# Performance work log

Hardware: AMD Instinct MI355X
Metric: run time of the kernel (lower is better)

Reference implementation:

```python
import jax, jax.numpy as jnp
import numpy as np

B, L, DM, H = 1, 2048, 3072, 24
D = DM // H            # 128 head dim
MLP = 4 * DM           # 12288
EPS = 1e-6


def setup_inputs() -> dict:
    key = jax.random.key(0)
    ks = jax.random.split(key, 12)
    s = lambda fan_in: 1.0 / np.sqrt(fan_in)
    return {
        "x": jax.random.normal(ks[0], (B, L, DM), jnp.float32),
        "vec": jax.random.normal(ks[1], (B, DM), jnp.float32),
        "pe": jax.random.normal(ks[2], (1, 1, L, D // 2, 2, 2), jnp.float32),
        # Modulation linear: dim -> 3*dim
        "mod_w": jax.random.normal(ks[3], (DM, 3 * DM), jnp.float32) * s(DM),
        "mod_b": jnp.zeros((3 * DM,), jnp.float32),
        # linear1: dim -> 3*dim + mlp
        "lin1_w": jax.random.normal(ks[4], (DM, 3 * DM + MLP), jnp.float32) * s(DM),
        "lin1_b": jnp.zeros((3 * DM + MLP,), jnp.float32),
        # linear2: dim + mlp -> dim
        "lin2_w": jax.random.normal(ks[5], (DM + MLP, DM), jnp.float32) * s(DM + MLP),
        "lin2_b": jnp.zeros((DM,), jnp.float32),
        # QKNorm RMS scales (per head_dim)
        "q_scale": jnp.ones((D,), jnp.float32),
        "k_scale": jnp.ones((D,), jnp.float32),
    }


def _rms_norm(t, scale):
    # RMSNorm over last dim (head_dim), eps 1e-6
    rrms = jax.lax.rsqrt(jnp.mean(jnp.square(t), axis=-1, keepdims=True) + EPS)
    return t * rrms * scale


def _apply_rope(t, pe):
    # t: (B,H,L,D); pe: (1,1,L,D/2,2,2) as in flux apply_rope
    t2 = t.reshape(B, H, L, D // 2, 1, 2)
    out = pe[..., 0] * t2[..., 0] + pe[..., 1] * t2[..., 1]  # (B,H,L,D/2,2)
    return out.reshape(B, H, L, D)


def reference(x, vec, pe, mod_w, mod_b, lin1_w, lin1_b, lin2_w, lin2_b, q_scale, k_scale):
    # Modulation: Linear(silu(vec)) -> shift, scale, gate, each (B,1,DM)
    mod = jax.nn.silu(vec) @ mod_w + mod_b
    shift, scale, gate = jnp.split(mod[:, None, :], 3, axis=-1)

    # pre_norm: LayerNorm without affine, eps 1e-6
    mu = jnp.mean(x, axis=-1, keepdims=True)
    var = jnp.mean(jnp.square(x - mu), axis=-1, keepdims=True)
    xn = (x - mu) * jax.lax.rsqrt(var + EPS)
    x_mod = (1.0 + scale) * xn + shift

    # fused QKV + MLP projection
    h = x_mod @ lin1_w + lin1_b
    qkv, mlp = h[..., : 3 * DM], h[..., 3 * DM :]
    qkv = qkv.reshape(B, L, 3, H, D).transpose(2, 0, 3, 1, 4)  # (3,B,H,L,D)
    q, k, v = qkv[0], qkv[1], qkv[2]

    q = _rms_norm(q, q_scale)
    k = _rms_norm(k, k_scale)
    q = _apply_rope(q, pe)
    k = _apply_rope(k, pe)

    # scaled dot-product attention (non-causal, SDPA default scale)
    scores = jnp.einsum("bhqd,bhkd->bhqk", q, k) * (1.0 / np.sqrt(D))
    attn = jax.nn.softmax(scores, axis=-1)
    o = jnp.einsum("bhqk,bhkd->bhqd", attn, v)
    o = o.transpose(0, 2, 1, 3).reshape(B, L, DM)  # B H L D -> B L (H D)

    out = jnp.concatenate([o, jax.nn.gelu(mlp, approximate=True)], axis=-1) @ lin2_w + lin2_b
    return x + gate * out
```

## Files before the change

### kernel.cpp

```cpp
#include <hip/hip_runtime.h>
#include <math.h>

#define LQ 2048
#define DMODEL 3072
#define NHEADS 24
#define DHEADC 128
#define NQKV 9216
#define NOUT1 21504
#define KIN2 15360
#define EPSV 1e-6f

typedef __attribute__((ext_vector_type(8))) short short8;
typedef __attribute__((ext_vector_type(4))) short short4v;
typedef __attribute__((ext_vector_type(4))) float f32x4;

__device__ __forceinline__ short f2bf(float f) {
  unsigned int u = __float_as_uint(f);
  unsigned int r = (u + 0x7fffu + ((u >> 16) & 1u)) >> 16;
  return (short)(unsigned short)r;
}

__device__ __forceinline__ float geluf(float v) {
  float inner = 0.7978845608028654f * (v + 0.044715f * v * v * v);
  return 0.5f * v * (1.0f + tanhf(inner));
}

__device__ __forceinline__ void async_ld16(void* lds, const void* g) {
  __builtin_amdgcn_global_load_lds(
      (const __attribute__((address_space(1))) unsigned int*)g,
      (__attribute__((address_space(3))) unsigned int*)lds, 16, 0, 0);
}

__global__ __launch_bounds__(256) void k_wconv(const float* __restrict__ w,
                                               short* __restrict__ wt,
                                               int K, int N) {
  __shared__ float tile[32][33];
  int bk = blockIdx.x * 32, bn = blockIdx.y * 32;
  int t = threadIdx.x;
  int r = t >> 3, c = (t & 7) * 4;
  float4 v = *reinterpret_cast<const float4*>(w + (size_t)(bk + r) * N + bn + c);
  tile[r][c + 0] = v.x; tile[r][c + 1] = v.y; tile[r][c + 2] = v.z; tile[r][c + 3] = v.w;
  __syncthreads();
  short4v o;
  o[0] = f2bf(tile[c + 0][r]); o[1] = f2bf(tile[c + 1][r]);
  o[2] = f2bf(tile[c + 2][r]); o[3] = f2bf(tile[c + 3][r]);
  *reinterpret_cast<short4v*>(wt + (size_t)(bn + r) * K + bk + c) = o;
}

__global__ __launch_bounds__(256) void k_modpart(const float* __restrict__ vec,
                                                 const float* __restrict__ mod_w,
                                                 float* __restrict__ partial) {
  __shared__ float sv[128];
  int t = threadIdx.x;
  int nb = blockIdx.x * 256;
  int kb = blockIdx.y * 128;
  if (t < 128) { float z = vec[kb + t]; sv[t] = z / (1.0f + expf(-z)); }
  __syncthreads();
  const float* wp = mod_w + (size_t)kb * NQKV + nb + t;
  float acc = 0.0f;
#pragma unroll 8
  for (int k = 0; k < 128; k++) acc += sv[k] * wp[(size_t)k * NQKV];
  partial[(size_t)blockIdx.y * NQKV + nb + t] = acc;
}

__global__ __launch_bounds__(256) void k_modred(const float* __restrict__ partial,
                                                const float* __restrict__ mod_b,
                                                float* __restrict__ modv) {
  int n = blockIdx.x * 256 + threadIdx.x;
  float acc = mod_b[n];
#pragma unroll
  for (int ky = 0; ky < 24; ky++) acc += partial[(size_t)ky * NQKV + n];
  modv[n] = acc;
}

__global__ __launch_bounds__(256) void k_ln(const float* __restrict__ x,
                                            const float* __restrict__ modv,
                                            short* __restrict__ xmod) {
  int l = blockIdx.x, t = threadIdx.x;
  const float* xr = x + (size_t)l * DMODEL;
  const float4* xr4 = (const float4*)xr;
  float4 vbuf[3];
  float s = 0.f, ss = 0.f;
#pragma unroll
  for (int i = 0; i < 3; i++) {
    float4 v = xr4[t + i * 256];
    vbuf[i] = v;
    s += v.x + v.y + v.z + v.w;
    ss += v.x * v.x + v.y * v.y + v.z * v.z + v.w * v.w;
  }
#pragma unroll
  for (int m = 32; m >= 1; m >>= 1) { s += __shfl_xor(s, m); ss += __shfl_xor(ss, m); }
  __shared__ float red[8];
  __shared__ float stats[2];
  int wave = t >> 6;
  if ((t & 63) == 0) { red[wave] = s; red[4 + wave] = ss; }
  __syncthreads();
  if (t == 0) {
    float st = red[0] + red[1] + red[2] + red[3];
    float sst = red[4] + red[5] + red[6] + red[7];
    float mu = st / DMODEL;
    float var = sst / DMODEL - mu * mu;
    stats[0] = mu; stats[1] = rsqrtf(var + EPSV);
  }
  __syncthreads();
  float mu = stats[0], rr = stats[1];
#pragma unroll
  for (int i = 0; i < 3; i++) {
    float4 v = vbuf[i];
    int c = (t + i * 256) * 4;
    short4v o;
    o[0] = f2bf((1.f + modv[DMODEL + c + 0]) * ((v.x - mu) * rr) + modv[c + 0]);
    o[1] = f2bf((1.f + modv[DMODEL + c + 1]) * ((v.y - mu) * rr) + modv[c + 1]);
    o[2] = f2bf((1.f + modv[DMODEL + c + 2]) * ((v.z - mu) * rr) + modv[c + 2]);
    o[3] = f2bf((1.f + modv[DMODEL + c + 3]) * ((v.w - mu) * rr) + modv[c + 3]);
    *(short4v*)(xmod + (size_t)l * DMODEL + c) = o;
  }
}

__global__ __launch_bounds__(256) void k_gemm1(const short* __restrict__ A,
                                               const short* __restrict__ Bt,
                                               const float* __restrict__ bias,
                                               float* __restrict__ qraw,
                                               float* __restrict__ kraw,
                                               short* __restrict__ vt,
                                               short* __restrict__ a2) {
  __shared__ __align__(16) short As[128 * 32];
  __shared__ __align__(16) short Bs[128 * 32];
  const int K = DMODEL;
  int t = threadIdx.x;
  int bm = blockIdx.x * 128, bn = blockIdx.y * 128;
  int wave = t >> 6, lane = t & 63;
  int wm = (wave >> 1) * 64, wn = (wave & 1) * 64;
  int lrow = lane & 15, lko = (lane >> 4) * 8;
  int srow = wave * 16 + (lane >> 2);
  int scol = (lane & 3) * 8;
  const short* ga0 = A + (size_t)(bm + srow) * K + scol;
  const short* ga1 = ga0 + (size_t)64 * K;
  const short* gb0 = Bt + (size_t)(bn + srow) * K + scol;
  const short* gb1 = gb0 + (size_t)64 * K;
  short* la0 = As + wave * 512;
  short* la1 = As + 64 * 32 + wave * 512;
  short* lb0 = Bs + wave * 512;
  short* lb1 = Bs + 64 * 32 + wave * 512;
  f32x4 zero = {0.f, 0.f, 0.f, 0.f};
  f32x4 acc[4][4];
#pragma unroll
  for (int i = 0; i < 4; i++)
#pragma unroll
    for (int j = 0; j < 4; j++) acc[i][j] = zero;
  for (int k0 = 0; k0 < K; k0 += 32) {
    __syncthreads();
    async_ld16(la0, ga0 + k0);
    async_ld16(la1, ga1 + k0);
    async_ld16(lb0, gb0 + k0);
    async_ld16(lb1, gb1 + k0);
    __syncthreads();
    short8 af[4], bfr[4];
#pragma unroll
    for (int i = 0; i < 4; i++) af[i] = *(const short8*)&As[(wm + i * 16 + lrow) * 32 + lko];
#pragma unroll
    for (int j = 0; j < 4; j++) bfr[j] = *(const short8*)&Bs[(wn + j * 16 + lrow) * 32 + lko];
#pragma unroll
    for (int i = 0; i < 4; i++)
#pragma unroll
      for (int j = 0; j < 4; j++)
        acc[i][j] = __builtin_amdgcn_mfma_f32_16x16x32_bf16(af[i], bfr[j], acc[i][j], 0, 0, 0);
  }
  int r0 = bm + wm + ((lane >> 4) << 2);
  int c0 = bn + wn + lrow;
#pragma unroll
  for (int j = 0; j < 4; j++) {
    int col = c0 + j * 16;
    float bb = bias[col];
#pragma unroll
    for (int i = 0; i < 4; i++) {
#pragma unroll
      for (int r = 0; r < 4; r++) {
        float v = acc[i][j][r] + bb;
        int row = r0 + i * 16 + r;
        if (col < NQKV) {
          int s = col / DMODEL;
          int rem = col - s * DMODEL;
          int hh = rem >> 7, d = rem & 127;
          if (s == 0)      qraw[((size_t)hh * LQ + row) * DHEADC + d] = v;
          else if (s == 1) kraw[((size_t)hh * LQ + row) * DHEADC + d] = v;
          else             vt[((size_t)hh * DHEADC + d) * LQ + row] = f2bf(v);
        } else {
          a2[(size_t)row * KIN2 + DMODEL + (col - NQKV)] = f2bf(geluf(v));
        }
      }
    }
  }
}

__global__ __launch_bounds__(256) void k_qkprep(const float* __restrict__ qraw,
                                                const float* __restrict__ kraw,
                                                const float* __restrict__ pe,
                                                const float* __restrict__ q_scale,
                                                const float* __restrict__ k_scale,
                                                short* __restrict__ qn,
                                                short* __restrict__ kn) {
  int wave = threadIdx.x >> 6, lane = threadIdx.x & 63;
  int l = blockIdx.x * 4 + wave;
  int h = blockIdx.y;
  int isK = blockIdx.z;
  const float* src = (isK ? kraw : qraw) + ((size_t)h * LQ + l) * DHEADC;
  const float* sc  = isK ? k_scale : q_scale;
  short* dst = (isK ? kn : qn) + ((size_t)h * LQ + l) * DHEADC;
  float2 tv = *(const float2*)(src + lane * 2);
  float ssq = tv.x * tv.x + tv.y * tv.y;
#pragma unroll
  for (int m = 1; m < 64; m <<= 1) ssq += __shfl_xor(ssq, m);
  float rr = rsqrtf(ssq * (1.0f / 128.0f) + EPSV);
  float t0 = tv.x * rr * sc[lane * 2];
  float t1 = tv.y * rr * sc[lane * 2 + 1];
  float4 p4 = *(const float4*)(pe + ((size_t)l * 64 + lane) * 4);
  float o0 = p4.x * t0 + p4.y * t1;
  float o1 = p4.z * t0 + p4.w * t1;
  if (!isK) { o0 *= 0.08838834764831845f; o1 *= 0.08838834764831845f; }
  dst[lane * 2] = f2bf(o0);
  dst[lane * 2 + 1] = f2bf(o1);
}

__global__ __launch_bounds__(256) void k_flash(const short* __restrict__ qn,
                                               const short* __restrict__ kn,
                                               const short* __restrict__ vt,
                                               short* __restrict__ a2) {
  __shared__ short Qs[128][136];
  __shared__ short Ks[32][136];
  __shared__ short Vs[128][40];
  __shared__ short Ps[4][32][40];
  int t = threadIdx.x;
  int qb = blockIdx.x * 128, h = blockIdx.y;
  int wave = t >> 6, lane = t & 63;
  int lrow = lane & 15, lko = (lane >> 4) * 8;
  int wm = wave * 32;
  const short* qbase = qn + ((size_t)h * LQ + qb) * DHEADC;
#pragma unroll
  for (int i = 0; i < 8; i++) {
    int idx = i * 256 + t;
    int row = idx >> 4, c = (idx & 15) * 8;
    *(short8*)&Qs[row][c] = *(const short8*)(qbase + (size_t)row * DHEADC + c);
  }
  f32x4 zero = {0.f, 0.f, 0.f, 0.f};
  f32x4 oacc[2][8];
#pragma unroll
  for (int i = 0; i < 2; i++)
#pragma unroll
    for (int j = 0; j < 8; j++) oacc[i][j] = zero;
  float mI[2][4], lI[2][4];
#pragma unroll
  for (int i = 0; i < 2; i++)
#pragma unroll
    for (int r = 0; r < 4; r++) { mI[i][r] = -1e30f; lI[i][r] = 0.f; }
  __syncthreads();
  for (int kt = 0; kt < 64; kt++) {
    int krow0 = kt * 32;
#pragma unroll
    for (int i = 0; i < 2; i++) {
      int idx = i * 256 + t;
      int row = idx >> 4, c = (idx & 15) * 8;
      *(short8*)&Ks[row][c] = *(const short8*)(kn + ((size_t)h * LQ + krow0 + row) * DHEADC + c);
    }
#pragma unroll
    for (int i = 0; i < 2; i++) {
      int idx = i * 256 + t;
      int d = idx >> 2, c = (idx & 3) * 8;
      *(short8*)&Vs[d][c] = *(const short8*)(vt + ((size_t)h * DHEADC + d) * LQ + krow0 + c);
    }
    __syncthreads();
    f32x4 sacc[2][2];
#pragma unroll
    for (int i = 0; i < 2; i++)
#pragma unroll
      for (int j = 0; j < 2; j++) sacc[i][j] = zero;
#pragma unroll
    for (int kk = 0; kk < 4; kk++) {
      short8 qa[2], kb[2];
#pragma unroll
      for (int i = 0; i < 2; i++) qa[i] = *(const short8*)&Qs[wm + i * 16 + lrow][kk * 32 + lko];
#pragma unroll
      for (int j = 0; j < 2; j++) kb[j] = *(const short8*)&Ks[j * 16 + lrow][kk * 32 + lko];
#pragma unroll
      for (int i = 0; i < 2; i++)
#pragma unroll
        for (int j = 0; j < 2; j++)
          sacc[i][j] = __builtin_amdgcn_mfma_f32_16x16x32_bf16(qa[i], kb[j], sacc[i][j], 0, 0, 0);
    }
#pragma unroll
    for (int i = 0; i < 2; i++) {
      float al[4];
#pragma unroll
      for (int r = 0; r < 4; r++) {
        float mx = fmaxf(sacc[i][0][r], sacc[i][1][r]);
#pragma unroll
        for (int m = 1; m < 16; m <<= 1) mx = fmaxf(mx, __shfl_xor(mx, m));
        float mnew = fmaxf(mI[i][r], mx);
        float alpha = exp2f((mI[i][r] - mnew) * 1.4426950408889634f);
        float p0 = exp2f((sacc[i][0][r] - mnew) * 1.4426950408889634f);
        float p1 = exp2f((sacc[i][1][r] - mnew) * 1.4426950408889634f);
        sacc[i][0][r] = p0; sacc[i][1][r] = p1;
        float rs = p0 + p1;
#pragma unroll
        for (int m = 1; m < 16; m <<= 1) rs += __shfl_xor(rs, m);
        lI[i][r] = lI[i][r] * alpha + rs;
        mI[i][r] = mnew;
        al[r] = alpha;
      }
#pragma unroll
      for (int j = 0; j < 8; j++) {
        f32x4 o = oacc[i][j];
        o[0] *= al[0]; o[1] *= al[1]; o[2] *= al[2]; o[3] *= al[3];
        oacc[i][j] = o;
      }
#pragma unroll
      for (int j = 0; j < 2; j++)
#pragma unroll
        for (int r = 0; r < 4; r++)
          Ps[wave][i * 16 + (lane >> 4) * 4 + r][j * 16 + lrow] = f2bf(sacc[i][j][r]);
    }
    short8 pa[2];
#pragma unroll
    for (int i = 0; i < 2; i++) pa[i] = *(const short8*)&Ps[wave][i * 16 + lrow][lko];
#pragma unroll
    for (int j = 0; j < 8; j++) {
      short8 vb = *(const short8*)&Vs[j * 16 + lrow][lko];
#pragma unroll
      for (int i = 0; i < 2; i++)
        oacc[i][j] = __builtin_amdgcn_mfma_f32_16x16x32_bf16(pa[i], vb, oacc[i][j], 0, 0, 0);
    }
    __syncthreads();
  }
#pragma unroll
  for (int i = 0; i < 2; i++) {
    float inv[4];
#pragma unroll
    for (int r = 0; r < 4; r++) inv[r] = 1.0f / lI[i][r];
#pragma unroll
    for (int j = 0; j < 8; j++) {
#pragma unroll
      for (int r = 0; r < 4; r++) {
        int row = qb + wm + i * 16 + (lane >> 4) * 4 + r;
        int col = h * DHEADC + j * 16 + lrow;
        a2[(size_t)row * KIN2 + col] = f2bf(oacc[i][j][r] * inv[r]);
      }
    }
  }
}

__global__ __launch_bounds__(256) void k_gemm2(const short* __restrict__ A,
                                               const short* __restrict__ Bt,
                                               const float* __restrict__ bias,
                                               const float* __restrict__ x,
                                               const float* __restrict__ gate,
                                               float* __restrict__ out) {
  __shared__ __align__(16) short As[128 * 32];
  __shared__ __align__(16) short Bs[128 * 32];
  const int K = KIN2;
  int t = threadIdx.x;
  int bm = blockIdx.x * 128, bn = blockIdx.y * 128;
  int wave = t >> 6, lane = t & 63;
  int wm = (wave >> 1) * 64, wn = (wave & 1) * 64;
  int lrow = lane & 15, lko = (lane >> 4) * 8;
  int srow = wave * 16 + (lane >> 2);
  int scol = (lane & 3) * 8;
  const short* ga0 = A + (size_t)(bm + srow) * K + scol;
  const short* ga1 = ga0 + (size_t)64 * K;
  const short* gb0 = Bt + (size_t)(bn + srow) * K + scol;
  const short* gb1 = gb0 + (size_t)64 * K;
  short* la0 = As + wave * 512;
  short* la1 = As + 64 * 32 + wave * 512;
  short* lb0 = Bs + wave * 512;
  short* lb1 = Bs + 64 * 32 + wave * 512;
  f32x4 zero = {0.f, 0.f, 0.f, 0.f};
  f32x4 acc[4][4];
#pragma unroll
  for (int i = 0; i < 4; i++)
#pragma unroll
    for (int j = 0; j < 4; j++) acc[i][j] = zero;
  for (int k0 = 0; k0 < K; k0 += 32) {
    __syncthreads();
    async_ld16(la0, ga0 + k0);
    async_ld16(la1, ga1 + k0);
    async_ld16(lb0, gb0 + k0);
    async_ld16(lb1, gb1 + k0);
    __syncthreads();
    short8 af[4], bfr[4];
#pragma unroll
    for (int i = 0; i < 4; i++) af[i] = *(const short8*)&As[(wm + i * 16 + lrow) * 32 + lko];
#pragma unroll
    for (int j = 0; j < 4; j++) bfr[j] = *(const short8*)&Bs[(wn + j * 16 + lrow) * 32 + lko];
#pragma unroll
    for (int i = 0; i < 4; i++)
#pragma unroll
      for (int j = 0; j < 4; j++)
        acc[i][j] = __builtin_amdgcn_mfma_f32_16x16x32_bf16(af[i], bfr[j], acc[i][j], 0, 0, 0);
  }
  int r0 = bm + wm + ((lane >> 4) << 2);
  int c0 = bn + wn + lrow;
#pragma unroll
  for (int j = 0; j < 4; j++) {
    int col = c0 + j * 16;
    float bb = bias[col];
    float g = gate[col];
#pragma unroll
    for (int i = 0; i < 4; i++) {
#pragma unroll
      for (int r = 0; r < 4; r++) {
        int row = r0 + i * 16 + r;
        float v = acc[i][j][r] + bb;
        out[(size_t)row * DMODEL + col] = x[(size_t)row * DMODEL + col] + g * v;
      }
    }
  }
}

extern "C" void kernel_launch(void* const* d_in, const int* in_sizes, int n_in,
                              void* d_out, int out_size, void* d_ws, size_t ws_size,
                              hipStream_t stream) {
  (void)in_sizes; (void)n_in; (void)out_size; (void)ws_size;
  const float* x       = (const float*)d_in[0];
  const float* vec     = (const float*)d_in[1];
  const float* pe      = (const float*)d_in[2];
  const float* mod_w   = (const float*)d_in[3];
  const float* mod_b   = (const float*)d_in[4];
  const float* lin1_w  = (const float*)d_in[5];
  const float* lin1_b  = (const float*)d_in[6];
  const float* lin2_w  = (const float*)d_in[7];
  const float* lin2_b  = (const float*)d_in[8];
  const float* q_scale = (const float*)d_in[9];
  const float* k_scale = (const float*)d_in[10];
  float* out = (float*)d_out;

  char* base = (char*)d_ws;
  size_t off = 0;
  auto carve = [&](size_t bytes) -> void* {
    void* q = base + off;
    off += (bytes + 255) & ~(size_t)255;
    return q;
  };
  short* W1t  = (short*)carve((size_t)NOUT1 * DMODEL * 2);
  short* xmod = (short*)carve((size_t)LQ * DMODEL * 2);
  float* qraw = (float*)carve((size_t)NHEADS * LQ * DHEADC * 4);
  float* kraw = (float*)carve((size_t)NHEADS * LQ * DHEADC * 4);
  short* qnb  = (short*)carve((size_t)NHEADS * LQ * DHEADC * 2);
  short* knb  = (short*)carve((size_t)NHEADS * LQ * DHEADC * 2);
  short* vtb  = (short*)carve((size_t)NHEADS * LQ * DHEADC * 2);
  short* a2   = (short*)carve((size_t)LQ * KIN2 * 2);
  float* modv = (float*)carve((size_t)NQKV * 4);
  float* part = (float*)carve((size_t)24 * NQKV * 4);

  k_wconv<<<dim3(DMODEL / 32, NOUT1 / 32), 256, 0, stream>>>(lin1_w, W1t, DMODEL, NOUT1);
  k_modpart<<<dim3(NQKV / 256, 24), 256, 0, stream>>>(vec, mod_w, part);
  k_modred<<<NQKV / 256, 256, 0, stream>>>(part, mod_b, modv);
  k_ln<<<LQ, 256, 0, stream>>>(x, modv, xmod);
  k_gemm1<<<dim3(LQ / 128, NOUT1 / 128), 256, 0, stream>>>(xmod, W1t, lin1_b, qraw, kraw, vtb, a2);
  k_wconv<<<dim3(KIN2 / 32, DMODEL / 32), 256, 0, stream>>>(lin2_w, W1t, KIN2, DMODEL);
  k_qkprep<<<dim3(LQ / 4, NHEADS, 2), 256, 0, stream>>>(qraw, kraw, pe, q_scale, k_scale, qnb, knb);
  k_flash<<<dim3(LQ / 128, NHEADS), 256, 0, stream>>>(qnb, knb, vtb, a2);
  k_gemm2<<<dim3(LQ / 128, DMODEL / 128), 256, 0, stream>>>(a2, W1t, lin2_b, x, modv + 2 * DMODEL, out);
}
```

Before: 1.704 ms.

## Replace first GEMM with 256x256 double-buffered 8-wave pipelined kernel

Rewrites the QKV+MLP projection GEMM to use 256x256 tiles with 512 threads, a K-step of 64, and double-buffered LDS. Global-to-LDS async loads for later tiles are interleaved with MFMA phases, using explicit waitcnt, barriers and setprio. An XOR swizzle is applied to LDS addresses and the block index is remapped across the grid. This aims to hide memory latency, cut LDS bank conflicts and raise data reuse per tile. The cost is higher register and LDS pressure and a fragile hand-scheduled pipeline.

```diff
diff --git a/kernel.cpp b/kernel.cpp
--- a/kernel.cpp
+++ b/kernel.cpp
@@ -117,67 +117,160 @@
   }
 }
 
-__global__ __launch_bounds__(256) void k_gemm1(const short* __restrict__ A,
-                                               const short* __restrict__ Bt,
-                                               const float* __restrict__ bias,
-                                               float* __restrict__ qraw,
-                                               float* __restrict__ kraw,
-                                               short* __restrict__ vt,
-                                               short* __restrict__ a2) {
-  __shared__ __align__(16) short As[128 * 32];
-  __shared__ __align__(16) short Bs[128 * 32];
-  const int K = DMODEL;
+#define G1_NT 48
+#define G1_NITER 24
+
+__device__ __forceinline__ void ldA4(short8 af[4][2], const short* ldsA, int rbase,
+                                     int lrow, const int* kOff) {
+#pragma unroll
+  for (int m = 0; m < 4; m++)
+#pragma unroll
+    for (int ks = 0; ks < 2; ks++)
+      af[m][ks] = *(const short8*)&ldsA[(rbase + m * 16 + lrow) * 64 + kOff[ks]];
+}
+
+__device__ __forceinline__ void ldB2(short8 bfr[2][2], const short* ldsB, int rbase,
+                                     int lrow, const int* kOff) {
+#pragma unroll
+  for (int n = 0; n < 2; n++)
+#pragma unroll
+    for (int ks = 0; ks < 2; ks++)
+      bfr[n][ks] = *(const short8*)&ldsB[(rbase + n * 16 + lrow) * 64 + kOff[ks]];
+}
+
+__device__ __forceinline__ void stage_halfA(short* ldsT, const short* G, int rowbase,
+                                            int tauB, int half, int wid, int srow, int sk) {
+#pragma unroll
+  for (int c = 0; c < 2; c++) {
+    int j = c * 8 + wid;
+    int row0 = ((j >> 3) << 7) + half * 64 + ((j & 7) << 3);
+    const char* src = (const char*)G +
+                      (size_t)(rowbase + row0 + srow) * (size_t)(DMODEL * 2) + tauB + sk;
+    async_ld16(ldsT + row0 * 64, src);
+  }
+}
+
+__device__ __forceinline__ void stage_halfB(short* ldsT, const short* G, int rowbase,
+                                            int tauB, int half, int wid, int srow, int sk) {
+#pragma unroll
+  for (int c = 0; c < 2; c++) {
+    int j = c * 8 + wid;
+    int row0 = ((j >> 2) << 6) + half * 32 + ((j & 3) << 3);
+    const char* src = (const char*)G +
+                      (size_t)(rowbase + row0 + srow) * (size_t)(DMODEL * 2) + tauB + sk;
+    async_ld16(ldsT + row0 * 64, src);
+  }
+}
+
+#define SYNC_MFMA(mh, nh, VM)                                                       \
+  do {                                                                              \
+    if (VM) asm volatile("s_waitcnt vmcnt(6)" ::: "memory");                        \
+    __builtin_amdgcn_s_barrier();                                                   \
+    asm volatile("s_waitcnt lgkmcnt(0)" ::: "memory");                              \
+    __builtin_amdgcn_sched_barrier(0);                                              \
+    __builtin_amdgcn_s_setprio(1);                                                  \
+    _Pragma("unroll") for (int m_ = 0; m_ < 4; m_++)                                \
+      _Pragma("unroll") for (int n_ = 0; n_ < 2; n_++)                              \
+        _Pragma("unroll") for (int k_ = 0; k_ < 2; k_++)                            \
+          acc[(mh) * 4 + m_][(nh) * 2 + n_] =                                       \
+              __builtin_amdgcn_mfma_f32_16x16x32_bf16(                              \
+                  af[m_][k_], bfr[n_][k_], acc[(mh) * 4 + m_][(nh) * 2 + n_], 0, 0, 0); \
+    __builtin_amdgcn_s_setprio(0);                                                  \
+    __builtin_amdgcn_s_barrier();                                                   \
+  } while (0)
+
+#define G1_TB(tt) ((((tt) < G1_NT) ? (tt) : (G1_NT - 1)) * 128)
+
+__global__ __launch_bounds__(512, 2) void k_gemm1_8p(const short* __restrict__ A,
+                                                     const short* __restrict__ Bt,
+                                                     const float* __restrict__ bias,
+                                                     float* __restrict__ qraw,
+                                                     float* __restrict__ kraw,
+                                                     short* __restrict__ vt,
+                                                     short* __restrict__ a2) {
+  __shared__ __align__(16) short lds[2][2][256 * 64];
   int t = threadIdx.x;
-  int bm = blockIdx.x * 128, bn = blockIdx.y * 128;
-  int wave = t >> 6, lane = t & 63;
-  int wm = (wave >> 1) * 64, wn = (wave & 1) * 64;
-  int lrow = lane & 15, lko = (lane >> 4) * 8;
-  int srow = wave * 16 + (lane >> 2);
-  int scol = (lane & 3) * 8;
-  const short* ga0 = A + (size_t)(bm + srow) * K + scol;
-  const short* ga1 = ga0 + (size_t)64 * K;
-  const short* gb0 = Bt + (size_t)(bn + srow) * K + scol;
-  const short* gb1 = gb0 + (size_t)64 * K;
-  short* la0 = As + wave * 512;
-  short* la1 = As + 64 * 32 + wave * 512;
-  short* lb0 = Bs + wave * 512;
-  short* lb1 = Bs + 64 * 32 + wave * 512;
+  int wid = t >> 6, lane = t & 63;
+  int bid = blockIdx.x;
+  int swzb = (bid & 7) * 84 + (bid >> 3);
+  int bm = (swzb & 7) << 8;
+  int bn = (swzb >> 3) << 8;
+  int wm_ = (wid >> 2) << 7;
+  int wn_ = (wid & 3) << 6;
+  int lrow = lane & 15;
+  int swzx = (lane & 7) << 4;
+  int kOff[2];
+#pragma unroll
+  for (int ks = 0; ks < 2; ks++) kOff[ks] = ((ks * 64 + (lane >> 4) * 16) ^ swzx) >> 1;
+  int srow = lane >> 3;
+  int sk = ((lane & 7) * 16) ^ (srow << 4);
+
+  short* A0p = &lds[0][0][0];
+  short* B0p = &lds[0][1][0];
+  short* A1p = &lds[1][0][0];
+  short* B1p = &lds[1][1][0];
+
   f32x4 zero = {0.f, 0.f, 0.f, 0.f};
-  f32x4 acc[4][4];
-#pragma unroll
-  for (int i = 0; i < 4; i++)
+  f32x4 acc[8][4];
+#pragma unroll
+  for (int i = 0; i < 8; i++)
 #pragma unroll
     for (int j = 0; j < 4; j++) acc[i][j] = zero;
-  for (int k0 = 0; k0 < K; k0 += 32) {
-    __syncthreads();
-    async_ld16(la0, ga0 + k0);
-    async_ld16(la1, ga1 + k0);
-    async_ld16(lb0, gb0 + k0);
-    async_ld16(lb1, gb1 + k0);
-    __syncthreads();
-    short8 af[4], bfr[4];
-#pragma unroll
-    for (int i = 0; i < 4; i++) af[i] = *(const short8*)&As[(wm + i * 16 + lrow) * 32 + lko];
-#pragma unroll
-    for (int j = 0; j < 4; j++) bfr[j] = *(const short8*)&Bs[(wn + j * 16 + lrow) * 32 + lko];
-#pragma unroll
-    for (int i = 0; i < 4; i++)
-#pragma unroll
-      for (int j = 0; j < 4; j++)
-        acc[i][j] = __builtin_amdgcn_mfma_f32_16x16x32_bf16(af[i], bfr[j], acc[i][j], 0, 0, 0);
-  }
-  int r0 = bm + wm + ((lane >> 4) << 2);
-  int c0 = bn + wn + lrow;
-#pragma unroll
-  for (int j = 0; j < 4; j++) {
-    int col = c0 + j * 16;
+  short8 af[4][2], bfr[2][2];
+
+  stage_halfA(A0p, A, bm, 0, 0, wid, srow, sk);
+  stage_halfA(A0p, A, bm, 0, 1, wid, srow, sk);
+  stage_halfB(B0p, Bt, bn, 0, 0, wid, srow, sk);
+  stage_halfB(B0p, Bt, bn, 0, 1, wid, srow, sk);
+  stage_halfA(A1p, A, bm, 128, 0, wid, srow, sk);
+  stage_halfB(B1p, Bt, bn, 128, 1, wid, srow, sk);
+  stage_halfA(A1p, A, bm, 128, 1, wid, srow, sk);
+  asm volatile("s_waitcnt vmcnt(6)" ::: "memory");
+  __builtin_amdgcn_s_barrier();
+
+#pragma unroll 1
+  for (int it = 0; it < G1_NITER; ++it) {
+    int T = it * 2;
+    ldA4(af, A0p, wm_, lrow, kOff);
+    ldB2(bfr, B0p, wn_, lrow, kOff);
+    stage_halfB(B1p, Bt, bn, G1_TB(T + 1), 0, wid, srow, sk);
+    SYNC_MFMA(0, 0, 0);
+    ldB2(bfr, B0p, wn_ + 32, lrow, kOff);
+    stage_halfA(A0p, A, bm, G1_TB(T + 2), 0, wid, srow, sk);
+    SYNC_MFMA(0, 1, 0);
+    ldA4(af, A0p, wm_ + 64, lrow, kOff);
+    stage_halfB(B0p, Bt, bn, G1_TB(T + 2), 1, wid, srow, sk);
+    SYNC_MFMA(1, 1, 0);
+    ldB2(bfr, B0p, wn_, lrow, kOff);
+    stage_halfA(A0p, A, bm, G1_TB(T + 2), 1, wid, srow, sk);
+    SYNC_MFMA(1, 0, 1);
+    ldA4(af, A1p, wm_, lrow, kOff);
+    ldB2(bfr, B1p, wn_, lrow, kOff);
+    stage_halfB(B0p, Bt, bn, G1_TB(T + 2), 0, wid, srow, sk);
+    SYNC_MFMA(0, 0, 0);
+    ldB2(bfr, B1p, wn_ + 32, lrow, kOff);
+    stage_halfA(A1p, A, bm, G1_TB(T + 3), 0, wid, srow, sk);
+    SYNC_MFMA(0, 1, 0);
+    ldA4(af, A1p, wm_ + 64, lrow, kOff);
+    stage_halfB(B1p, Bt, bn, G1_TB(T + 3), 1, wid, srow, sk);
+    SYNC_MFMA(1, 1, 0);
+    ldB2(bfr, B1p, wn_, lrow, kOff);
+    stage_halfA(A1p, A, bm, G1_TB(T + 3), 1, wid, srow, sk);
+    SYNC_MFMA(1, 0, 1);
+  }
+
+  int r0 = bm + wm_ + ((lane >> 4) << 2);
+  int c0 = bn + wn_ + lrow;
+#pragma unroll
+  for (int an = 0; an < 4; an++) {
+    int col = c0 + an * 16;
     float bb = bias[col];
 #pragma unroll
-    for (int i = 0; i < 4; i++) {
+    for (int am = 0; am < 8; am++) {
 #pragma unroll
       for (int r = 0; r < 4; r++) {
-        float v = acc[i][j][r] + bb;
-        int row = r0 + i * 16 + r;
+        float v = acc[am][an][r] + bb;
+        int row = r0 + am * 16 + r;
         if (col < NQKV) {
           int s = col / DMODEL;
           int rem = col - s * DMODEL;
@@ -454,7 +547,8 @@
   k_modpart<<<dim3(NQKV / 256, 24), 256, 0, stream>>>(vec, mod_w, part);
   k_modred<<<NQKV / 256, 256, 0, stream>>>(part, mod_b, modv);
   k_ln<<<LQ, 256, 0, stream>>>(x, modv, xmod);
-  k_gemm1<<<dim3(LQ / 128, NOUT1 / 128), 256, 0, stream>>>(xmod, W1t, lin1_b, qraw, kraw, vtb, a2);
+  k_gemm1_8p<<<dim3((LQ / 256) * (NOUT1 / 256)), 512, 0, stream>>>(xmod, W1t, lin1_b,
+                                                                   qraw, kraw, vtb, a2);
   k_wconv<<<dim3(KIN2 / 32, DMODEL / 32), 256, 0, stream>>>(lin2_w, W1t, KIN2, DMODEL);
   k_qkprep<<<dim3(LQ / 4, NHEADS, 2), 256, 0, stream>>>(qraw, kraw, pe, q_scale, k_scale, qnb, knb);
   k_flash<<<dim3(LQ / 128, NHEADS), 256, 0, stream>>>(qnb, knb, vtb, a2);
```

After: 1.628 ms. -4.5%, faster.
